# Performance work log

Measured on AMD Instinct MI355X. Metric: run time of the kernel, lower is better.

## Reference

```python
import jax, jax.numpy as jnp
import numpy as np

H = 512       # num_hidden == num_cell
D_IN = 10     # input_dim (hardcoded by view(batch,10) in the original forward)
C = 10        # num_classes
B = 256       # batch
T = 256       # seq_length


def setup_inputs() -> dict:
    key = jax.random.key(0)
    ks = jax.random.split(key, 16)

    def xavier(k, shape):
        fan_in, fan_out = shape[1], shape[0]
        limit = np.sqrt(6.0 / (fan_in + fan_out))
        return jax.random.uniform(k, shape, jnp.float32, -limit, limit)

    inp = {"x": jax.random.normal(ks[0], (B, T, D_IN), jnp.float32)}
    names_shapes = [
        ("w_gx", (H, D_IN)), ("w_gh", (H, H)), ("b_g", (H, 1)),
        ("w_ix", (H, D_IN)), ("w_ih", (H, H)), ("b_i", (H, 1)),
        ("w_fx", (H, D_IN)), ("w_fh", (H, H)), ("b_f", (H, 1)),
        ("w_ox", (H, D_IN)), ("w_oh", (H, H)), ("b_o", (H, 1)),
        ("w_out", (C, H)),
    ]
    for (name, shape), k in zip(names_shapes, ks[1:14]):
        inp[name] = xavier(k, shape)
    inp["b_out"] = jnp.ones((C, 1), jnp.float32)  # original leaves b_out at ones
    return inp


def reference(x, w_gx, w_gh, b_g, w_ix, w_ih, b_i, w_fx, w_fh, b_f,
              w_ox, w_oh, b_o, w_out, b_out):
    batch = x.shape[0]
    # time-major, transposed inputs: [T, D_IN, B] to match w @ cur_input layout
    xs = jnp.transpose(x, (1, 2, 0))

    def step(carry, xt):
        h, c = carry  # [H, B] each
        g = jnp.tanh(w_gx @ xt + w_gh @ h + b_g)
        i = jax.nn.sigmoid(w_ix @ xt + w_ih @ h + b_i)
        f = jax.nn.sigmoid(w_fx @ xt + w_fh @ h + b_f)
        o = jax.nn.sigmoid(w_ox @ xt + w_oh @ h + b_o)
        c_new = g * i + c * f
        h_new = jnp.tanh(c_new) * o
        return (h_new, c_new), None

    h0 = jnp.zeros((H, batch), x.dtype)
    c0 = jnp.zeros((H, batch), x.dtype)
    (h, _), _ = jax.lax.scan(step, (h0, c0), xs)

    p = w_out @ h + b_out              # [C, B]
    return jax.nn.softmax(p, axis=0).T  # [B, C]
```

## Files before the change

### kernel.cpp

```cpp
#include <hip/hip_runtime.h>


#define Hdim 512
#define Bdim 256
#define Tdim 256
#define Kpad 544
#define LROW 552
#define PROW 520
#define LDS_BYTES ((64 * LROW * 2 + 16 * PROW + 512) * 2)

typedef __bf16 bf16x8 __attribute__((ext_vector_type(8)));
typedef float f32x4 __attribute__((ext_vector_type(4)));
typedef unsigned long long u64;

__device__ __forceinline__ unsigned short f2bf(float f) {
    union { float f; unsigned u; } x; x.f = f;
    unsigned r = x.u + 0x7FFFu + ((x.u >> 16) & 1u);
    return (unsigned short)(r >> 16);
}
__device__ __forceinline__ float bf2f(unsigned short h) {
    union { unsigned u; float f; } x; x.u = ((unsigned)h) << 16;
    return x.f;
}
__device__ __forceinline__ bf16x8 ld8(const unsigned short* p) {
    return *reinterpret_cast<const bf16x8*>(p);
}
__device__ __forceinline__ u64 ldA(const u64* p) {
    return __hip_atomic_load(p, __ATOMIC_RELAXED, __HIP_MEMORY_SCOPE_AGENT);
}
__device__ __forceinline__ void stH32(unsigned* p, unsigned v) {
    __hip_atomic_store(p, v, __ATOMIC_RELAXED, __HIP_MEMORY_SCOPE_AGENT);
}
__device__ __forceinline__ f32x4 mfma16(bf16x8 a, bf16x8 b, f32x4 c) {
    return __builtin_amdgcn_mfma_f32_16x16x32_bf16(a, b, c, 0, 0, 0);
}
__device__ __forceinline__ bf16x8 pack2(u64 a, u64 b) {
    union { u64 q[2]; bf16x8 v; } u; u.q[0] = a; u.q[1] = b; return u.v;
}
__device__ __forceinline__ float sigm(float x) { return 1.f / (1.f + __expf(-x)); }
__device__ __forceinline__ float tanh_fast(float x) {
    return 2.f / (1.f + __expf(-2.f * x)) - 1.f;
}

__global__ void k_prep_w(const float* __restrict__ w_gh, const float* __restrict__ w_ih,
                         const float* __restrict__ w_fh, const float* __restrict__ w_oh,
                         const float* __restrict__ w_gx, const float* __restrict__ w_ix,
                         const float* __restrict__ w_fx, const float* __restrict__ w_ox,
                         unsigned short* __restrict__ Whi, unsigned short* __restrict__ Wlo) {
    int idx = blockIdx.x * 256 + threadIdx.x;
    if (idx >= 2048 * Kpad) return;
    int rw = idx / Kpad;
    int k  = idx % Kpad;
    int gate = rw & 3;
    int i = rw >> 2;
    float v = 0.f;
    if (k < 512) {
        const float* wh = (gate == 0) ? w_gh : (gate == 1) ? w_ih : (gate == 2) ? w_fh : w_oh;
        v = wh[i * 512 + k];
    } else if (k < 522) {
        const float* wx = (gate == 0) ? w_gx : (gate == 1) ? w_ix : (gate == 2) ? w_fx : w_ox;
        v = wx[i * 10 + (k - 512)];
    }
    unsigned short hi = f2bf(v);
    unsigned short lo = f2bf(v - bf2f(hi));
    Whi[idx] = hi;
    Wlo[idx] = lo;
}

__global__ void k_prep_x(const float* __restrict__ x,
                         unsigned short* __restrict__ Xhi, unsigned short* __restrict__ Xlo) {
    int idx = blockIdx.x * 256 + threadIdx.x;
    if (idx >= Tdim * Bdim * 32) return;
    int j = idx & 31;
    int b = (idx >> 5) & 255;
    int t = idx >> 13;
    float v = 0.f;
    if (j < 10) v = x[(b * Tdim + t) * 10 + j];
    unsigned short hi = f2bf(v);
    unsigned short lo = f2bf(v - bf2f(hi));
    Xhi[idx] = hi;
    Xlo[idx] = lo;
}

__global__ void k_zero(float* __restrict__ p) {
    p[blockIdx.x * 256 + threadIdx.x] = 0.f;
}

__global__ __launch_bounds__(256, 1) void k_persist(
    const unsigned short* __restrict__ Whi, const unsigned short* __restrict__ Wlo,
    const unsigned short* __restrict__ Xhi, const unsigned short* __restrict__ Xlo,
    unsigned short* H0c, unsigned short* H1c,
    float* __restrict__ Hf32,
    const float* __restrict__ bg, const float* __restrict__ bi,
    const float* __restrict__ bf_, const float* __restrict__ bo,
    unsigned* flags) {
    extern __shared__ unsigned short lds[];
    unsigned short* Lhi = lds;
    unsigned short* Llo = lds + 64 * LROW;
    unsigned short* Pp  = lds + 64 * LROW * 2;
    unsigned short* Ho  = Pp + 16 * PROW;

    const int bid = blockIdx.x;
    const int rg  = bid >> 3;
    const int m0  = rg * 64;
    const int ct  = bid & 7;
    const int bn0 = ct * 32;
    const int tid = threadIdx.x;
    const int lane = tid & 63;
    const int w  = tid >> 6;
    const int lr = lane & 15, q = lane >> 4;

    unsigned* myflag = flags + (((ct << 5) + rg) << 4);
    unsigned* pollp  = flags + (((ct << 5) + (lane & 31)) << 4);

    const int cl = tid >> 4;
    const int e  = tid & 15;

    for (int it = tid; it < 64 * 68; it += 256) {
        int r = it / 68, c8 = (it % 68) * 8;
        *(bf16x8*)&Lhi[r * LROW + c8] = ld8(Whi + (size_t)(m0 + r) * Kpad + c8);
        *(bf16x8*)&Llo[r * LROW + c8] = ld8(Wlo + (size_t)(m0 + r) * Kpad + c8);
    }
    __syncthreads();

    const int kq = q * 8;
    const int col0 = bn0 + lr;
    const int col1 = col0 + 16;
    const int i0 = rg * 16 + w * 4 + q;
    const int r16 = w * 4 + q;

    float c0 = 0.f, c1 = 0.f;
    const f32x4 binit = { bg[i0], bi[i0], bf_[i0], bo[i0] };

    const unsigned short* Ah = &Lhi[(w * 16 + lr) * LROW + kq];
    const unsigned short* Al = &Llo[(w * 16 + lr) * LROW + kq];
    const unsigned short* Bl = &Pp[lr * PROW + kq];
    unsigned short* Pd0 = &Pp[cl * PROW + e * 16];
    unsigned short* Pd1 = &Pp[cl * PROW + e * 16 + 256];

    const size_t myblk = ((size_t)ct * 32 + rg) * 512;

    for (int t = 0; t < Tdim; ++t) {
        const unsigned short* Rh = (t & 1) ? H1c : H0c;
        unsigned short* Whc = (t & 1) ? H0c : H1c;

        u64 a0[4], a1[4];
        {
            const u64* s0 = (const u64*)(Rh + (((size_t)ct * 32 + e) * 32 + cl) * 16);
            const u64* s1 = (const u64*)(Rh + (((size_t)ct * 32 + e + 16) * 32 + cl) * 16);
#pragma unroll
            for (int v = 0; v < 4; ++v) a0[v] = ldA(s0 + v);
#pragma unroll
            for (int v = 0; v < 4; ++v) a1[v] = ldA(s1 + v);
        }
        *(bf16x8*)(Pd0)     = pack2(a0[0], a0[1]);
        *(bf16x8*)(Pd0 + 8) = pack2(a0[2], a0[3]);
        *(bf16x8*)(Pd1)     = pack2(a1[0], a1[1]);
        *(bf16x8*)(Pd1 + 8) = pack2(a1[2], a1[3]);
        __syncthreads();

        u64 b0[4], b1[4];
        {
            const u64* s0 = (const u64*)(Rh + (((size_t)ct * 32 + e) * 32 + 16 + cl) * 16);
            const u64* s1 = (const u64*)(Rh + (((size_t)ct * 32 + e + 16) * 32 + 16 + cl) * 16);
#pragma unroll
            for (int v = 0; v < 4; ++v) b0[v] = ldA(s0 + v);
#pragma unroll
            for (int v = 0; v < 4; ++v) b1[v] = ldA(s1 + v);
        }
        const unsigned short* xb  = Xhi + ((size_t)t * Bdim) * 32;
        const unsigned short* xbl = Xlo + ((size_t)t * Bdim) * 32;
        bf16x8 xh0 = ld8(xb + col0 * 32 + kq), xl0 = ld8(xbl + col0 * 32 + kq);
        bf16x8 xh1 = ld8(xb + col1 * 32 + kq), xl1 = ld8(xbl + col1 * 32 + kq);

        f32x4 acc0 = binit, acc1 = binit;
#pragma unroll
        for (int kb = 0; kb < 16; ++kb) {
            const int k = kb * 32;
            bf16x8 ah = ld8(Ah + k), al = ld8(Al + k);
            bf16x8 bh = ld8(Bl + k);
            acc0 = mfma16(ah, bh, acc0);
            acc0 = mfma16(al, bh, acc0);
        }
        {
            bf16x8 ah = ld8(Ah + 512), al = ld8(Al + 512);
            acc0 = mfma16(ah, xh0, acc0);
            acc0 = mfma16(ah, xl0, acc0);
            acc0 = mfma16(al, xh0, acc0);
        }
        __syncthreads();

        *(bf16x8*)(Pd0)     = pack2(b0[0], b0[1]);
        *(bf16x8*)(Pd0 + 8) = pack2(b0[2], b0[3]);
        *(bf16x8*)(Pd1)     = pack2(b1[0], b1[1]);
        *(bf16x8*)(Pd1 + 8) = pack2(b1[2], b1[3]);
        __syncthreads();

#pragma unroll
        for (int kb = 0; kb < 16; ++kb) {
            const int k = kb * 32;
            bf16x8 ah = ld8(Ah + k), al = ld8(Al + k);
            bf16x8 bh = ld8(Bl + k);
            acc1 = mfma16(ah, bh, acc1);
            acc1 = mfma16(al, bh, acc1);
        }
        {
            bf16x8 ah = ld8(Ah + 512), al = ld8(Al + 512);
            acc1 = mfma16(ah, xh1, acc1);
            acc1 = mfma16(ah, xl1, acc1);
            acc1 = mfma16(al, xh1, acc1);
        }

        {
            float g = tanh_fast(acc0[0]), ii = sigm(acc0[1]);
            float f = sigm(acc0[2]),      o  = sigm(acc0[3]);
            c0 = g * ii + c0 * f;
            float h = tanh_fast(c0) * o;
            Ho[lr * 16 + r16] = f2bf(h);
            if (t == Tdim - 1) Hf32[(size_t)col0 * Hdim + i0] = h;
        }
        {
            float g = tanh_fast(acc1[0]), ii = sigm(acc1[1]);
            float f = sigm(acc1[2]),      o  = sigm(acc1[3]);
            c1 = g * ii + c1 * f;
            float h = tanh_fast(c1) * o;
            Ho[(16 + lr) * 16 + r16] = f2bf(h);
            if (t == Tdim - 1) Hf32[(size_t)col1 * Hdim + i0] = h;
        }
        __syncthreads();

        stH32((unsigned*)(Whc + myblk) + tid, *(const unsigned*)&Ho[tid * 2]);

        asm volatile("s_waitcnt vmcnt(0)" ::: "memory");
        __syncthreads();
        if (w == 0) {
            if (lane == 0)
                __hip_atomic_store(myflag, (unsigned)(t + 1),
                                   __ATOMIC_RELAXED, __HIP_MEMORY_SCOPE_AGENT);
            const unsigned tgt = (unsigned)(t + 1);
            bool ok = lane >= 32;
            int guard = 1 << 16;
            while (!ok && --guard) {
                unsigned v = __hip_atomic_load(pollp, __ATOMIC_RELAXED,
                                               __HIP_MEMORY_SCOPE_AGENT);
                ok = (v >= tgt);
                if (!ok) __builtin_amdgcn_s_sleep(1);
            }
        }
        __syncthreads();
        asm volatile("" ::: "memory");
    }
}

__global__ __launch_bounds__(64) void k_out(
    const float* __restrict__ Hf32, const float* __restrict__ w_out,
    const float* __restrict__ b_out, float* __restrict__ out) {
    int b = blockIdx.x;
    int lane = threadIdx.x;
    const f32x4* h4 = (const f32x4*)(Hf32 + (size_t)b * 512);
    f32x4 h0 = h4[lane * 2], h1 = h4[lane * 2 + 1];
    float acc[10];
#pragma unroll
    for (int c = 0; c < 10; ++c) {
        const f32x4* w4 = (const f32x4*)(w_out + c * 512);
        f32x4 w0 = w4[lane * 2], w1 = w4[lane * 2 + 1];
        acc[c] = h0[0]*w0[0] + h0[1]*w0[1] + h0[2]*w0[2] + h0[3]*w0[3]
               + h1[0]*w1[0] + h1[1]*w1[1] + h1[2]*w1[2] + h1[3]*w1[3];
    }
#pragma unroll
    for (int s = 32; s >= 1; s >>= 1)
#pragma unroll
        for (int c = 0; c < 10; ++c) acc[c] += __shfl_xor(acc[c], s, 64);
    if (lane == 0) {
        float logit[10];
#pragma unroll
        for (int c = 0; c < 10; ++c) logit[c] = acc[c] + b_out[c];
        float m = logit[0];
#pragma unroll
        for (int c = 1; c < 10; ++c) m = fmaxf(m, logit[c]);
        float e[10], sum = 0.f;
#pragma unroll
        for (int c = 0; c < 10; ++c) { e[c] = __expf(logit[c] - m); sum += e[c]; }
        float inv = 1.f / sum;
#pragma unroll
        for (int c = 0; c < 10; ++c) out[b * 10 + c] = e[c] * inv;
    }
}

extern "C" void kernel_launch(void* const* d_in, const int* in_sizes, int n_in,
                              void* d_out, int out_size, void* d_ws, size_t ws_size,
                              hipStream_t stream) {
    const float* x    = (const float*)d_in[0];
    const float* w_gx = (const float*)d_in[1];
    const float* w_gh = (const float*)d_in[2];
    const float* b_g  = (const float*)d_in[3];
    const float* w_ix = (const float*)d_in[4];
    const float* w_ih = (const float*)d_in[5];
    const float* b_i  = (const float*)d_in[6];
    const float* w_fx = (const float*)d_in[7];
    const float* w_fh = (const float*)d_in[8];
    const float* b_f  = (const float*)d_in[9];
    const float* w_ox = (const float*)d_in[10];
    const float* w_oh = (const float*)d_in[11];
    const float* b_o  = (const float*)d_in[12];
    const float* w_out = (const float*)d_in[13];
    const float* b_out = (const float*)d_in[14];
    float* out = (float*)d_out;

    char* ws = (char*)d_ws;
    size_t off = 0;
    auto alloc = [&](size_t bytes) { void* p = ws + off; off += (bytes + 255) & ~255ull; return p; };
    unsigned*       flags = (unsigned*)alloc(16384);
    unsigned short* H0c   = (unsigned short*)alloc((size_t)Bdim * 512 * 2);
    unsigned short* H1c   = (unsigned short*)alloc((size_t)Bdim * 512 * 2);
    float*          Hf32  = (float*)alloc((size_t)Bdim * 512 * 4);
    unsigned short* Whi   = (unsigned short*)alloc(2048ull * Kpad * 2);
    unsigned short* Wlo   = (unsigned short*)alloc(2048ull * Kpad * 2);
    unsigned short* Xhi   = (unsigned short*)alloc((size_t)Tdim * Bdim * 32 * 2);
    unsigned short* Xlo   = (unsigned short*)alloc((size_t)Tdim * Bdim * 32 * 2);
    (void)ws_size; (void)in_sizes; (void)n_in; (void)out_size;

    k_prep_w<<<(2048 * Kpad + 255) / 256, 256, 0, stream>>>(
        w_gh, w_ih, w_fh, w_oh, w_gx, w_ix, w_fx, w_ox, Whi, Wlo);
    k_prep_x<<<(Tdim * Bdim * 32 + 255) / 256, 256, 0, stream>>>(x, Xhi, Xlo);
    k_zero<<<272, 256, 0, stream>>>((float*)flags);

    hipFuncSetAttribute((const void*)k_persist,
                        hipFuncAttributeMaxDynamicSharedMemorySize, LDS_BYTES);
    k_persist<<<dim3(256), dim3(256), LDS_BYTES, stream>>>(
        Whi, Wlo, Xhi, Xlo, H0c, H1c,
        Hf32, b_g, b_i, b_f, b_o, flags);

    k_out<<<256, 64, 0, stream>>>(Hf32, w_out, b_out, out);
}
```

Baseline: 1.350 ms.

## Split per-step grid barrier into two half-flag phases to overlap sync with compute

Each block now publishes its hidden-state output in two halves, each with its own flag array. Consumers wait only on the half they need before loading each slice of h. The first column tile's gate math and store are moved ahead of the second tile's MFMA loop, so publishing, flag polling and loading overlap with the remaining compute instead of sitting behind one end-of-step barrier. The explicit vmcnt wait before the flag store is removed, which relies on __syncthreads for ordering and risks visibility races. The flag buffer and zeroing kernel grow to match.

```diff
diff --git a/kernel.cpp b/kernel.cpp
--- a/kernel.cpp
+++ b/kernel.cpp
@@ -40,6 +40,19 @@
 __device__ __forceinline__ float sigm(float x) { return 1.f / (1.f + __expf(-x)); }
 __device__ __forceinline__ float tanh_fast(float x) {
     return 2.f / (1.f + __expf(-2.f * x)) - 1.f;
+}
+__device__ __forceinline__ void pollFlags(const unsigned* pollp, unsigned tgt, int lane) {
+    bool ok = lane >= 32;
+    if (!ok) {
+        unsigned v = __hip_atomic_load(pollp, __ATOMIC_RELAXED, __HIP_MEMORY_SCOPE_AGENT);
+        ok = (v >= tgt);
+    }
+    int guard = 1 << 16;
+    while (!ok && --guard) {
+        __builtin_amdgcn_s_sleep(1);
+        unsigned v = __hip_atomic_load(pollp, __ATOMIC_RELAXED, __HIP_MEMORY_SCOPE_AGENT);
+        ok = (v >= tgt);
+    }
 }
 
 __global__ void k_prep_w(const float* __restrict__ w_gh, const float* __restrict__ w_ih,
@@ -110,8 +123,12 @@
     const int w  = tid >> 6;
     const int lr = lane & 15, q = lane >> 4;
 
-    unsigned* myflag = flags + (((ct << 5) + rg) << 4);
-    unsigned* pollp  = flags + (((ct << 5) + (lane & 31)) << 4);
+    unsigned* flagsA = flags;
+    unsigned* flagsB = flags + 4096;
+    unsigned* myflagA = flagsA + (((ct << 5) + rg) << 4);
+    unsigned* myflagB = flagsB + (((ct << 5) + rg) << 4);
+    const unsigned* pollpA = flagsA + (((ct << 5) + (lane & 31)) << 4);
+    const unsigned* pollpB = flagsB + (((ct << 5) + (lane & 31)) << 4);
 
     const int cl = tid >> 4;
     const int e  = tid & 15;
@@ -143,6 +160,11 @@
     for (int t = 0; t < Tdim; ++t) {
         const unsigned short* Rh = (t & 1) ? H1c : H0c;
         unsigned short* Whc = (t & 1) ? H0c : H1c;
+        const unsigned tgt = (unsigned)t;
+
+        if (w == 0) pollFlags(pollpA, tgt, lane);
+        __syncthreads();
+        asm volatile("" ::: "memory");
 
         u64 a0[4], a1[4];
         {
@@ -152,26 +174,30 @@
             for (int v = 0; v < 4; ++v) a0[v] = ldA(s0 + v);
 #pragma unroll
             for (int v = 0; v < 4; ++v) a1[v] = ldA(s1 + v);
+        }
+        const unsigned short* xb  = Xhi + ((size_t)t * Bdim) * 32;
+        const unsigned short* xbl = Xlo + ((size_t)t * Bdim) * 32;
+        bf16x8 xh0 = ld8(xb + col0 * 32 + kq), xl0 = ld8(xbl + col0 * 32 + kq);
+        bf16x8 xh1 = ld8(xb + col1 * 32 + kq), xl1 = ld8(xbl + col1 * 32 + kq);
+
+        if (w == 0) pollFlags(pollpB, tgt, lane);
+        __syncthreads();
+        asm volatile("" ::: "memory");
+
+        u64 b0[4], b1[4];
+        {
+            const u64* s0 = (const u64*)(Rh + (((size_t)ct * 32 + e) * 32 + 16 + cl) * 16);
+            const u64* s1 = (const u64*)(Rh + (((size_t)ct * 32 + e + 16) * 32 + 16 + cl) * 16);
+#pragma unroll
+            for (int v = 0; v < 4; ++v) b0[v] = ldA(s0 + v);
+#pragma unroll
+            for (int v = 0; v < 4; ++v) b1[v] = ldA(s1 + v);
         }
         *(bf16x8*)(Pd0)     = pack2(a0[0], a0[1]);
         *(bf16x8*)(Pd0 + 8) = pack2(a0[2], a0[3]);
         *(bf16x8*)(Pd1)     = pack2(a1[0], a1[1]);
         *(bf16x8*)(Pd1 + 8) = pack2(a1[2], a1[3]);
         __syncthreads();
-
-        u64 b0[4], b1[4];
-        {
-            const u64* s0 = (const u64*)(Rh + (((size_t)ct * 32 + e) * 32 + 16 + cl) * 16);
-            const u64* s1 = (const u64*)(Rh + (((size_t)ct * 32 + e + 16) * 32 + 16 + cl) * 16);
-#pragma unroll
-            for (int v = 0; v < 4; ++v) b0[v] = ldA(s0 + v);
-#pragma unroll
-            for (int v = 0; v < 4; ++v) b1[v] = ldA(s1 + v);
-        }
-        const unsigned short* xb  = Xhi + ((size_t)t * Bdim) * 32;
-        const unsigned short* xbl = Xlo + ((size_t)t * Bdim) * 32;
-        bf16x8 xh0 = ld8(xb + col0 * 32 + kq), xl0 = ld8(xbl + col0 * 32 + kq);
-        bf16x8 xh1 = ld8(xb + col1 * 32 + kq), xl1 = ld8(xbl + col1 * 32 + kq);
 
         f32x4 acc0 = binit, acc1 = binit;
 #pragma unroll
@@ -188,6 +214,14 @@
             acc0 = mfma16(ah, xl0, acc0);
             acc0 = mfma16(al, xh0, acc0);
         }
+        {
+            float g = tanh_fast(acc0[0]), ii = sigm(acc0[1]);
+            float f = sigm(acc0[2]),      o  = sigm(acc0[3]);
+            c0 = g * ii + c0 * f;
+            float h = tanh_fast(c0) * o;
+            Ho[lr * 16 + r16] = f2bf(h);
+            if (t == Tdim - 1) Hf32[(size_t)col0 * Hdim + i0] = h;
+        }
         __syncthreads();
 
         *(bf16x8*)(Pd0)     = pack2(b0[0], b0[1]);
@@ -195,6 +229,9 @@
         *(bf16x8*)(Pd1)     = pack2(b1[0], b1[1]);
         *(bf16x8*)(Pd1 + 8) = pack2(b1[2], b1[3]);
         __syncthreads();
+
+        if (tid < 128)
+            stH32((unsigned*)(Whc + myblk) + tid, *(const unsigned*)&Ho[tid * 2]);
 
 #pragma unroll
         for (int kb = 0; kb < 16; ++kb) {
@@ -210,15 +247,6 @@
             acc1 = mfma16(ah, xl1, acc1);
             acc1 = mfma16(al, xh1, acc1);
         }
-
-        {
-            float g = tanh_fast(acc0[0]), ii = sigm(acc0[1]);
-            float f = sigm(acc0[2]),      o  = sigm(acc0[3]);
-            c0 = g * ii + c0 * f;
-            float h = tanh_fast(c0) * o;
-            Ho[lr * 16 + r16] = f2bf(h);
-            if (t == Tdim - 1) Hf32[(size_t)col0 * Hdim + i0] = h;
-        }
         {
             float g = tanh_fast(acc1[0]), ii = sigm(acc1[1]);
             float f = sigm(acc1[2]),      o  = sigm(acc1[3]);
@@ -228,27 +256,16 @@
             if (t == Tdim - 1) Hf32[(size_t)col1 * Hdim + i0] = h;
         }
         __syncthreads();
-
-        stH32((unsigned*)(Whc + myblk) + tid, *(const unsigned*)&Ho[tid * 2]);
-
-        asm volatile("s_waitcnt vmcnt(0)" ::: "memory");
-        __syncthreads();
-        if (w == 0) {
-            if (lane == 0)
-                __hip_atomic_store(myflag, (unsigned)(t + 1),
-                                   __ATOMIC_RELAXED, __HIP_MEMORY_SCOPE_AGENT);
-            const unsigned tgt = (unsigned)(t + 1);
-            bool ok = lane >= 32;
-            int guard = 1 << 16;
-            while (!ok && --guard) {
-                unsigned v = __hip_atomic_load(pollp, __ATOMIC_RELAXED,
-                                               __HIP_MEMORY_SCOPE_AGENT);
-                ok = (v >= tgt);
-                if (!ok) __builtin_amdgcn_s_sleep(1);
-            }
-        }
-        __syncthreads();
-        asm volatile("" ::: "memory");
+        if (tid == 0)
+            __hip_atomic_store(myflagA, (unsigned)(t + 1),
+                               __ATOMIC_RELAXED, __HIP_MEMORY_SCOPE_AGENT);
+
+        if (tid >= 128)
+            stH32((unsigned*)(Whc + myblk) + tid, *(const unsigned*)&Ho[tid * 2]);
+        __syncthreads();
+        if (tid == 0)
+            __hip_atomic_store(myflagB, (unsigned)(t + 1),
+                               __ATOMIC_RELAXED, __HIP_MEMORY_SCOPE_AGENT);
     }
 }
 
@@ -310,7 +327,7 @@
     char* ws = (char*)d_ws;
     size_t off = 0;
     auto alloc = [&](size_t bytes) { void* p = ws + off; off += (bytes + 255) & ~255ull; return p; };
-    unsigned*       flags = (unsigned*)alloc(16384);
+    unsigned*       flags = (unsigned*)alloc(32768);
     unsigned short* H0c   = (unsigned short*)alloc((size_t)Bdim * 512 * 2);
     unsigned short* H1c   = (unsigned short*)alloc((size_t)Bdim * 512 * 2);
     float*          Hf32  = (float*)alloc((size_t)Bdim * 512 * 4);
@@ -323,7 +340,7 @@
     k_prep_w<<<(2048 * Kpad + 255) / 256, 256, 0, stream>>>(
         w_gh, w_ih, w_fh, w_oh, w_gx, w_ix, w_fx, w_ox, Whi, Wlo);
     k_prep_x<<<(Tdim * Bdim * 32 + 255) / 256, 256, 0, stream>>>(x, Xhi, Xlo);
-    k_zero<<<272, 256, 0, stream>>>((float*)flags);
+    k_zero<<<288, 256, 0, stream>>>((float*)flags);
 
     hipFuncSetAttribute((const void*)k_persist,
                         hipFuncAttributeMaxDynamicSharedMemorySize, LDS_BYTES);
```

Result: faster. 1.111 ms (median of 2 runs) (-17.7%).
